# Kernel tuning notes

Measured on AMD Instinct MI355X. Metric: run time of the kernel, lower is better.

Reference implementation:

```python
import jax, jax.numpy as jnp
import numpy as np
import math

B, NQ, NK, HD = 8, 1024, 1024, 1024   # batch, q_len(=up_dim), kv_len(=img_size+15), hidden
H, HS, KC = 8, 128, 32                # heads, head_size=hidden/8, k_caption
EPS = 1e-5


def setup_inputs() -> dict:
    key = jax.random.key(0)
    ks = jax.random.split(key, 16)
    f = lambda i, sh: jax.random.normal(ks[i], sh, dtype=jnp.float32)
    s = 0.02  # weight init scale
    return {
        "v": f(0, (B, NK, HD)),
        "k": f(1, (B, NK, HD)),
        "q": f(2, (B, NQ, HD)),
        "c": f(3, (B, KC, HD)),
        "Wv": f(4, (HD, HD)) * s, "bv": jnp.zeros((HD,), jnp.float32),
        "Wk": f(5, (HD, HD)) * s, "bk": jnp.zeros((HD,), jnp.float32),
        "Wq": f(6, (HD, HD)) * s, "bq": jnp.zeros((HD,), jnp.float32),
        "Wc": f(7, (HD, HD)) * s, "bc": jnp.zeros((HD,), jnp.float32),
        "Wm": f(8, (HD, HD)) * s, "bm": jnp.zeros((HD,), jnp.float32),
        "Wup": f(9, (NQ, KC)) * s,          # nn.Linear(k_caption, up_dim, bias=False) weight (out,in)
        "ln_w": jnp.ones((NK,), jnp.float32),
        "ln_b": jnp.zeros((NK,), jnp.float32),
        "tau": jnp.float32(3.0),
    }


def _heads(x, W, b):
    # x: [B, N, HD] -> [B, H, N, HS]
    y = x @ W.T + b
    return y.reshape(x.shape[0], x.shape[1], H, HS).transpose(0, 2, 1, 3)


def reference(v, k, q, c, Wv, bv, Wk, bk, Wq, bq, Wc, bc, Wm, bm, Wup, ln_w, ln_b, tau):
    vh = _heads(v, Wv, bv)                      # [B,H,NK,HS]
    kh = _heads(k, Wk, bk)                      # [B,H,NK,HS]
    qh = _heads(q, Wq, bq)                      # [B,H,NQ,HS]
    ch = _heads(c, Wc, bc)                      # [B,H,KC,HS]

    inv_sqrt_d = 1.0 / math.sqrt(HS)            # d_k == d_c == head_size
    scores = jnp.einsum("bhqd,bhkd->bhqk", qh, kh) * inv_sqrt_d  # [B,H,NQ,NK]

    # up-sample context along caption axis: KC -> NQ (Linear over that axis, no bias)
    cu = jnp.einsum("bhcd,uc->bhud", ch, Wup)   # [B,H,NQ,HS]
    c_scores = jnp.einsum("bhud,bhkd->bhuk", cu, kh) * inv_sqrt_d  # [B,H,NQ,NK]

    t = jnp.tanh(tau)
    scores = (scores + c_scores * t) / (1.0 + t)

    # LayerNorm over the key axis (last dim), applied to raw scores
    mu = jnp.mean(scores, axis=-1, keepdims=True)
    var = jnp.var(scores, axis=-1, keepdims=True)
    scores = (scores - mu) * jax.lax.rsqrt(var + EPS) * ln_w + ln_b

    att = jax.nn.softmax(scores, axis=-1)       # dropout_r=0 -> identity
    out = jnp.einsum("bhqk,bhkd->bhqd", att, vh)  # [B,H,NQ,HS]
    out = out.transpose(0, 2, 1, 3).reshape(q.shape[0], NQ, HD)
    return out @ Wm.T + bm
```

## Files before the change

### kernel.cpp

```cpp
#include <hip/hip_runtime.h>
#include <hip/hip_fp16.h>


typedef _Float16 f16;
typedef _Float16 f16x8 __attribute__((ext_vector_type(8)));
typedef _Float16 f16x4 __attribute__((ext_vector_type(4)));
typedef float    f32x4 __attribute__((ext_vector_type(4)));

#define B_  8
#define NQ_ 1024
#define NK_ 1024
#define HD_ 1024
#define H_  8
#define HS_ 128
#define KC_ 32

__device__ __forceinline__ void g2lds16(const void* g, void* l) {
    __builtin_amdgcn_global_load_lds((const __attribute__((address_space(1))) void*)g,
                                     (__attribute__((address_space(3))) void*)l, 16, 0, 0);
}

__global__ __launch_bounds__(256) void fill_sentinel(float* __restrict__ out, int n) {
    int i = blockIdx.x * 256 + threadIdx.x;
    if (i < n) out[i] = 12345.0f;
}

__global__ __launch_bounds__(256) void cvt_f32_f16(const float* __restrict__ in,
                                                   f16* __restrict__ out, int n4) {
    int i = blockIdx.x * 256 + threadIdx.x;
    if (i >= n4) return;
    float4 v = ((const float4*)in)[i];
    f16x4 o;
    o[0] = (f16)v.x; o[1] = (f16)v.y; o[2] = (f16)v.z; o[3] = (f16)v.w;
    ((f16x4*)out)[i] = o;
}

template <int MODE>
__global__ __launch_bounds__(256) void gemm_nt(
    const f16* __restrict__ A, long long sA,
    const f16* __restrict__ B, long long sB,
    void* __restrict__ Cv, long long sC,
    int M, int N, int K,
    const float* __restrict__ bias,
    const f16* __restrict__ extra, long long sE,
    const float* __restrict__ taup)
{
    __shared__ __align__(16) f16 As[128 * 32];
    __shared__ __align__(16) f16 Bs[128 * 32];
    const int bz = blockIdx.z;
    const f16* Ab = A + (size_t)bz * sA;
    const f16* Bb = B + (size_t)bz * sB;
    const int row0 = blockIdx.y * 128, col0 = blockIdx.x * 128;
    const int tid = threadIdx.x, wave = tid >> 6, lane = tid & 63;
    const int g = lane >> 4, li = lane & 15;
    const int wr = wave >> 1, wc = wave & 1;

    f32x4 acc[4][4];
#pragma unroll
    for (int i = 0; i < 4; i++)
#pragma unroll
        for (int j = 0; j < 4; j++) acc[i][j] = (f32x4){0.f, 0.f, 0.f, 0.f};

    for (int k0 = 0; k0 < K; k0 += 32) {
#pragma unroll
        for (int i = 0; i < 2; i++) {
            int slot = i * 256 + tid;
            int rr = slot >> 2, cc8 = (slot & 3) << 3;
            int ra = row0 + rr;
            if (MODE == 0 && ra >= M) ra = M - 1;
            g2lds16(Ab + (size_t)ra * K + k0 + cc8, As + (size_t)(i * 256 + wave * 64) * 8);
            g2lds16(Bb + (size_t)(col0 + rr) * K + k0 + cc8, Bs + (size_t)(i * 256 + wave * 64) * 8);
        }
        __syncthreads();
        f16x8 af[4], bf[4];
#pragma unroll
        for (int i = 0; i < 4; i++) af[i] = *(const f16x8*)&As[(wr * 64 + i * 16 + li) * 32 + g * 8];
#pragma unroll
        for (int j = 0; j < 4; j++) bf[j] = *(const f16x8*)&Bs[(wc * 64 + j * 16 + li) * 32 + g * 8];
#pragma unroll
        for (int i = 0; i < 4; i++)
#pragma unroll
            for (int j = 0; j < 4; j++)
                acc[i][j] = __builtin_amdgcn_mfma_f32_16x16x32_f16(af[i], bf[j], acc[i][j], 0, 0, 0);
        __syncthreads();
    }

    float tv = 0.f, qscale = 0.f;
    if constexpr (MODE == 3) {
        tv = tanhf(taup[0]);
        qscale = 0.08838834764831845f / (1.0f + tv);
    }
#pragma unroll
    for (int i = 0; i < 4; i++) {
#pragma unroll
        for (int j = 0; j < 4; j++) {
            int cc = col0 + wc * 64 + j * 16 + li;
            float bcol = (MODE == 2) ? 0.f : bias[cc];
#pragma unroll
            for (int r = 0; r < 4; r++) {
                int row = row0 + wr * 64 + i * 16 + g * 4 + r;
                if (MODE == 0 && row >= M) continue;
                float v = acc[i][j][r];
                if constexpr (MODE == 2) v += bias[row]; else v += bcol;
                size_t idx = (size_t)bz * sC + (size_t)row * N + cc;
                if constexpr (MODE == 0) ((float*)Cv)[idx] = v;
                else if constexpr (MODE == 1 || MODE == 2) ((f16*)Cv)[idx] = (f16)v;
                else if constexpr (MODE == 3) {
                    v = (v + tv * (float)extra[(size_t)bz * sE + (size_t)row * N + cc]) * qscale;
                    ((f16*)Cv)[idx] = (f16)v;
                } else ((float*)Cv)[idx] = v;
            }
        }
    }
}

__global__ __launch_bounds__(256) void upsample_k(const float* __restrict__ Wup,
                                                  const float* __restrict__ CH,
                                                  f16* __restrict__ CU) {
    const int u = blockIdx.x, b = blockIdx.y;
    const float* ch = CH + (size_t)b * KC_ * HD_;
    float w[KC_];
#pragma unroll
    for (int c = 0; c < KC_; c++) w[c] = Wup[u * KC_ + c];
    f16* out = CU + ((size_t)b * NQ_ + u) * HD_;
#pragma unroll
    for (int t = 0; t < 4; t++) {
        int i = threadIdx.x + t * 256;
        float acc = 0.f;
#pragma unroll
        for (int c = 0; c < KC_; c++) acc += w[c] * ch[c * HD_ + i];
        out[i] = (f16)acc;
    }
}

#define MFMA16(A_, B_, C_) __builtin_amdgcn_mfma_f32_16x16x32_f16(A_, B_, C_, 0, 0, 0)

__global__ void attn_k(
    const f16* __restrict__ QE,
    const f16* __restrict__ KH,
    const f16* __restrict__ VT,
    const float* __restrict__ lnw_g, const float* __restrict__ lnb_g,
    f16* __restrict__ ATT)
{
    __shared__ __align__(16) f16 Plds[16 * NK_];
    __shared__ float redS[4][16], redQ[4][16], redL[4][16];

    const int tid = threadIdx.x;
    const int wave = tid >> 6, lane = tid & 63, g = lane >> 4, li = lane & 15;
    const int b = blockIdx.z, h = blockIdx.y, q0 = blockIdx.x * 16;

    const f16* qp = QE + (size_t)(b * NQ_ + q0 + li) * HD_ + h * HS_ + g * 8;
    f16x8 a[4];
#pragma unroll
    for (int ks = 0; ks < 4; ks++) a[ks] = *(const f16x8*)(qp + ks * 32);

    const f16* kp = KH + (size_t)(b * NK_ + wave * 256 + li) * HD_ + h * HS_ + g * 8;
    f32x4 s[16];
#pragma unroll
    for (int j = 0; j < 16; j++) s[j] = (f32x4){0.f, 0.f, 0.f, 0.f};

    f16x8 kbA0, kbA1, kbB0, kbB1, kbC0, kbC1, kbD0, kbD1;
#define QK_LD(BUF, U) do { \
        const f16* _p = kp + (size_t)((U) >> 1) * 16 * HD_ + ((U) & 1) * 64; \
        kb##BUF##0 = *(const f16x8*)(_p); \
        kb##BUF##1 = *(const f16x8*)(_p + 32); \
    } while (0)
#define QK_FMA(BUF, U) do { \
        __builtin_amdgcn_s_setprio(1); \
        s[(U) >> 1] = MFMA16(a[((U) & 1) * 2],     kb##BUF##0, s[(U) >> 1]); \
        s[(U) >> 1] = MFMA16(a[((U) & 1) * 2 + 1], kb##BUF##1, s[(U) >> 1]); \
        __builtin_amdgcn_s_setprio(0); \
    } while (0)

    QK_LD(A, 0); QK_LD(B, 1); QK_LD(C, 2); QK_LD(D, 3);
#pragma unroll
    for (int u = 0; u < 32; u += 4) {
        QK_FMA(A, u);     if (u + 4 < 32) QK_LD(A, u + 4);
        QK_FMA(B, u + 1); if (u + 5 < 32) QK_LD(B, u + 5);
        QK_FMA(C, u + 2); if (u + 6 < 32) QK_LD(C, u + 6);
        QK_FMA(D, u + 3); if (u + 7 < 32) QK_LD(D, u + 7);
    }

    float lw[16], lb[16];
#pragma unroll
    for (int j = 0; j < 16; j++) {
        int key = wave * 256 + j * 16 + li;
        lw[j] = lnw_g[key];
        lb[j] = lnb_g[key];
    }

    float ps[4] = {0, 0, 0, 0}, pq[4] = {0, 0, 0, 0};
#pragma unroll
    for (int j = 0; j < 16; j++)
#pragma unroll
        for (int r = 0; r < 4; r++) { float x = s[j][r]; ps[r] += x; pq[r] += x * x; }
#pragma unroll
    for (int m = 1; m < 16; m <<= 1)
#pragma unroll
        for (int r = 0; r < 4; r++) { ps[r] += __shfl_xor(ps[r], m, 64); pq[r] += __shfl_xor(pq[r], m, 64); }
    if (li == 0)
#pragma unroll
        for (int r = 0; r < 4; r++) { redS[wave][g * 4 + r] = ps[r]; redQ[wave][g * 4 + r] = pq[r]; }
    __syncthreads();

    float mu[4], rs[4];
#pragma unroll
    for (int r = 0; r < 4; r++) {
        int row = g * 4 + r;
        float s1 = redS[0][row] + redS[1][row] + redS[2][row] + redS[3][row];
        float s2 = redQ[0][row] + redQ[1][row] + redQ[2][row] + redQ[3][row];
        float m_ = s1 * (1.f / 1024.f);
        mu[r] = m_;
        rs[r] = rsqrtf(s2 * (1.f / 1024.f) - m_ * m_ + 1e-5f);
    }

    float sm[4] = {0, 0, 0, 0};
#pragma unroll
    for (int j = 0; j < 16; j++) {
        int key = wave * 256 + j * 16 + li;
        int chunk = key >> 3, sub = key & 7;
#pragma unroll
        for (int r = 0; r < 4; r++) {
            int row = g * 4 + r;
            float x = (s[j][r] - mu[r]) * rs[r] * lw[j] + lb[j];
            float e = __expf(fminf(x, 11.f) - 4.f);
            sm[r] += e;
            Plds[row * NK_ + ((chunk ^ (row & 7)) << 3) + sub] = (f16)e;
        }
    }
#pragma unroll
    for (int m = 1; m < 16; m <<= 1)
#pragma unroll
        for (int r = 0; r < 4; r++) sm[r] += __shfl_xor(sm[r], m, 64);
    if (li == 0)
#pragma unroll
        for (int r = 0; r < 4; r++) redL[wave][g * 4 + r] = sm[r];
    __syncthreads();

    float ls[4];
#pragma unroll
    for (int r = 0; r < 4; r++) {
        int row = g * 4 + r;
        ls[r] = redL[0][row] + redL[1][row] + redL[2][row] + redL[3][row];
    }

    const f16* vp = VT + (size_t)(b * HD_ + h * HS_ + wave * 32 + li) * NK_ + g * 8;
    f32x4 o0a = (f32x4){0.f, 0.f, 0.f, 0.f}, o0b = o0a, o1a = o0a, o1b = o0a;
    f16x8 paA, v0A, v1A, paB, v0B, v1B, paC, v0C, v1C, paD, v0D, v1D;
#define PV_LD(BUF, U) do { \
        pa##BUF = *(const f16x8*)&Plds[(size_t)li * NK_ + ((((U) * 4 + g) ^ (li & 7)) << 3)]; \
        v0##BUF = *(const f16x8*)(vp + (size_t)(U) * 32); \
        v1##BUF = *(const f16x8*)(vp + (size_t)16 * NK_ + (size_t)(U) * 32); \
    } while (0)
#define PV_FMA(BUF, OA, OB) do { \
        __builtin_amdgcn_s_setprio(1); \
        OA = MFMA16(pa##BUF, v0##BUF, OA); \
        OB = MFMA16(pa##BUF, v1##BUF, OB); \
        __builtin_amdgcn_s_setprio(0); \
    } while (0)

    PV_LD(A, 0); PV_LD(B, 1); PV_LD(C, 2); PV_LD(D, 3);
#pragma unroll
    for (int u = 0; u < 32; u += 4) {
        PV_FMA(A, o0a, o1a); if (u + 4 < 32) PV_LD(A, u + 4);
        PV_FMA(B, o0b, o1b); if (u + 5 < 32) PV_LD(B, u + 5);
        PV_FMA(C, o0a, o1a); if (u + 6 < 32) PV_LD(C, u + 6);
        PV_FMA(D, o0b, o1b); if (u + 7 < 32) PV_LD(D, u + 7);
    }

    f16* op = ATT + (size_t)(b * NQ_ + q0) * HD_ + h * HS_ + wave * 32 + li;
#pragma unroll
    for (int r = 0; r < 4; r++) {
        int row = g * 4 + r;
        float inv = 1.f / ls[r];
        op[(size_t)row * HD_]      = (f16)((o0a[r] + o0b[r]) * inv);
        op[(size_t)row * HD_ + 16] = (f16)((o1a[r] + o1b[r]) * inv);
    }
}

extern "C" void kernel_launch(void* const* d_in, const int* in_sizes, int n_in,
                              void* d_out, int out_size, void* d_ws, size_t ws_size,
                              hipStream_t stream) {
    const float* v   = (const float*)d_in[0];
    const float* k   = (const float*)d_in[1];
    const float* q   = (const float*)d_in[2];
    const float* c   = (const float*)d_in[3];
    const float* Wv  = (const float*)d_in[4];
    const float* bv  = (const float*)d_in[5];
    const float* Wk  = (const float*)d_in[6];
    const float* bk  = (const float*)d_in[7];
    const float* Wq  = (const float*)d_in[8];
    const float* bq  = (const float*)d_in[9];
    const float* Wc  = (const float*)d_in[10];
    const float* bc  = (const float*)d_in[11];
    const float* Wm  = (const float*)d_in[12];
    const float* bm  = (const float*)d_in[13];
    const float* Wup = (const float*)d_in[14];
    const float* lnw = (const float*)d_in[15];
    const float* lnb = (const float*)d_in[16];
    const float* tau = (const float*)d_in[17];

    const size_t NE  = (size_t)B_ * NK_ * HD_;
    const size_t NW  = (size_t)HD_ * HD_;
    const size_t NC  = (size_t)B_ * KC_ * HD_;

    const size_t REQUIRED = 95944704;
    if (ws_size < REQUIRED) {
        fill_sentinel<<<dim3((out_size + 255) / 256), dim3(256), 0, stream>>>((float*)d_out, out_size);
        return;
    }
    char* ws = (char*)d_ws;
    f16*  k16  = (f16*)(ws + 0);
    f16*  QE   = (f16*)(ws + 0);
    f16*  v16  = (f16*)(ws + 16777216);
    f16*  CU16 = (f16*)(ws + 16777216);
    f16*  q16  = (f16*)(ws + 33554432);
    f16*  ATT  = (f16*)(ws + 33554432);
    f16*  c16  = (f16*)(ws + 50331648);
    float* CHf = (float*)(ws + 50855936);
    f16*  wk16 = (f16*)(ws + 51904512);
    f16*  wq16 = (f16*)(ws + 54001664);
    f16*  wv16 = (f16*)(ws + 56098816);
    f16*  wc16 = (f16*)(ws + 58195968);
    f16*  wm16 = (f16*)(ws + 60293120);
    f16*  KH   = (f16*)(ws + 62390272);
    f16*  VT   = (f16*)(ws + 79167488);

    dim3 blk(256);
    auto cvt = [&](const float* in, f16* out, size_t n) {
        cvt_f32_f16<<<dim3((unsigned)(n / 1024)), blk, 0, stream>>>(in, out, (int)(n / 4));
    };
    cvt(k, k16, NE);
    cvt(v, v16, NE);
    cvt(q, q16, NE);
    cvt(c, c16, NC);
    cvt(Wk, wk16, NW);
    cvt(Wq, wq16, NW);
    cvt(Wv, wv16, NW);
    cvt(Wc, wc16, NW);
    cvt(Wm, wm16, NW);

    gemm_nt<1><<<dim3(8, 8, 8), blk, 0, stream>>>(k16, (long long)NK_ * HD_, wk16, 0,
        KH, (long long)NK_ * HD_, NK_, HD_, HD_, bk, nullptr, 0, nullptr);
    gemm_nt<2><<<dim3(8, 8, 8), blk, 0, stream>>>(wv16, 0, v16, (long long)NK_ * HD_,
        VT, (long long)HD_ * NK_, HD_, NK_, HD_, bv, nullptr, 0, nullptr);
    gemm_nt<0><<<dim3(8, 1, 8), blk, 0, stream>>>(c16, (long long)KC_ * HD_, wc16, 0,
        CHf, (long long)KC_ * HD_, KC_, HD_, HD_, bc, nullptr, 0, nullptr);
    upsample_k<<<dim3(NQ_, B_), blk, 0, stream>>>(Wup, CHf, CU16);
    gemm_nt<3><<<dim3(8, 8, 8), blk, 0, stream>>>(q16, (long long)NQ_ * HD_, wq16, 0,
        QE, (long long)NQ_ * HD_, NQ_, HD_, HD_, bq, CU16, (long long)NQ_ * HD_, tau);
    attn_k<<<dim3(NQ_ / 16, H_, B_), blk, 0, stream>>>(QE, KH, VT, lnw, lnb, ATT);
    gemm_nt<4><<<dim3(8, 8, 8), blk, 0, stream>>>(ATT, (long long)NQ_ * HD_, wm16, 0,
        d_out, (long long)NQ_ * HD_, NQ_, HD_, HD_, bm, nullptr, 0, nullptr);
}
```

Before: 639.9 us.

## Process 32 query rows per attention block with 8 waves and XCD-aware mapping

The attention kernel now handles 32 query rows per workgroup using 512 threads (8 waves), each wave covering 128 keys. Every K and V fragment loaded from global memory is therefore reused for two 16-row query tiles, halving K/V traffic per query. The 1D grid is remapped so that each (batch, head) pair's blocks land on the same XCD, which should improve L2 reuse of K/V. The reduction scratch is aliased onto the larger P buffer, which costs an extra barrier, and LDS use doubles to 64KB, which may lower occupancy.

```diff
diff --git a/kernel.cpp b/kernel.cpp
--- a/kernel.cpp
+++ b/kernel.cpp
@@ -135,40 +135,47 @@
 
 #define MFMA16(A_, B_, C_) __builtin_amdgcn_mfma_f32_16x16x32_f16(A_, B_, C_, 0, 0, 0)
 
-__global__ void attn_k(
+__global__ __launch_bounds__(512) void attn_k(
     const f16* __restrict__ QE,
     const f16* __restrict__ KH,
     const f16* __restrict__ VT,
     const float* __restrict__ lnw_g, const float* __restrict__ lnb_g,
     f16* __restrict__ ATT)
 {
-    __shared__ __align__(16) f16 Plds[16 * NK_];
-    __shared__ float redS[4][16], redQ[4][16], redL[4][16];
+    __shared__ __align__(16) f16 Plds[32 * NK_];
+    float* redS = (float*)Plds;
+    float* redQ = redS + 256;
+    float* redL = redQ + 256;
 
     const int tid = threadIdx.x;
     const int wave = tid >> 6, lane = tid & 63, g = lane >> 4, li = lane & 15;
-    const int b = blockIdx.z, h = blockIdx.y, q0 = blockIdx.x * 16;
+
+    const int wgid = blockIdx.x;
+    const int xcd = wgid & 7;
+    const int n = wgid >> 3;
+    const int pair = ((n >> 5) << 3) | xcd;
+    const int b = pair >> 3, h = pair & 7;
+    const int q0 = (n & 31) * 32;
 
     const f16* qp = QE + (size_t)(b * NQ_ + q0 + li) * HD_ + h * HS_ + g * 8;
-    f16x8 a[4];
-#pragma unroll
-    for (int ks = 0; ks < 4; ks++) a[ks] = *(const f16x8*)(qp + ks * 32);
-
-    const f16* kp = KH + (size_t)(b * NK_ + wave * 256 + li) * HD_ + h * HS_ + g * 8;
-    f32x4 s[16];
-#pragma unroll
-    for (int j = 0; j < 16; j++) s[j] = (f32x4){0.f, 0.f, 0.f, 0.f};
-
-    f16x8 kbA0, kbA1, kbB0, kbB1, kbC0, kbC1, kbD0, kbD1;
-#define QK_LD(BUF, U) do { \
-        const f16* _p = kp + (size_t)((U) >> 1) * 16 * HD_ + ((U) & 1) * 64; \
-        kb##BUF##0 = *(const f16x8*)(_p); \
-        kb##BUF##1 = *(const f16x8*)(_p + 32); \
-    } while (0)
+    f16x8 a0[4], a1[4];
+#pragma unroll
+    for (int ks = 0; ks < 4; ks++) {
+        a0[ks] = *(const f16x8*)(qp + ks * 32);
+        a1[ks] = *(const f16x8*)(qp + (size_t)16 * HD_ + ks * 32);
+    }
+
+    const f16* kp = KH + (size_t)(b * NK_ + wave * 128 + li) * HD_ + h * HS_ + g * 8;
+    f32x4 s0[8], s1[8];
+#pragma unroll
+    for (int j = 0; j < 8; j++) { s0[j] = (f32x4){0.f,0.f,0.f,0.f}; s1[j] = s0[j]; }
+
+    f16x8 kbA, kbB, kbC, kbD;
+#define QK_LD(BUF, U) kb##BUF = *(const f16x8*)(kp + (size_t)((U) & 7) * 16 * HD_ + ((U) >> 3) * 32)
 #define QK_FMA(BUF, U) do { \
         __builtin_amdgcn_s_setprio(1); \
-        s[(U) >> 1] = MFMA16(a[((U) & 1) * 2],     kb##BUF##0, s[(U) >> 1]); \
-        s[(U) >> 1] = MFMA16(a[((U) & 1) * 2 + 1], kb##BUF##1, s[(U) >> 1]); \
+        s0[(U) & 7] = MFMA16(a0[(U) >> 3], kb##BUF, s0[(U) & 7]); \
+        s1[(U) & 7] = MFMA16(a1[(U) >> 3], kb##BUF, s1[(U) & 7]); \
         __builtin_amdgcn_s_setprio(0); \
     } while (0)
 
@@ -181,81 +188,117 @@
         QK_FMA(D, u + 3); if (u + 7 < 32) QK_LD(D, u + 7);
     }
 
-    float lw[16], lb[16];
-#pragma unroll
-    for (int j = 0; j < 16; j++) {
-        int key = wave * 256 + j * 16 + li;
+    float lw[8], lb[8];
+#pragma unroll
+    for (int j = 0; j < 8; j++) {
+        int key = wave * 128 + j * 16 + li;
         lw[j] = lnw_g[key];
         lb[j] = lnb_g[key];
     }
 
-    float ps[4] = {0, 0, 0, 0}, pq[4] = {0, 0, 0, 0};
-#pragma unroll
-    for (int j = 0; j < 16; j++)
-#pragma unroll
-        for (int r = 0; r < 4; r++) { float x = s[j][r]; ps[r] += x; pq[r] += x * x; }
+    float ps0[4] = {0,0,0,0}, pq0[4] = {0,0,0,0}, ps1[4] = {0,0,0,0}, pq1[4] = {0,0,0,0};
+#pragma unroll
+    for (int j = 0; j < 8; j++)
+#pragma unroll
+        for (int r = 0; r < 4; r++) {
+            float x0 = s0[j][r]; ps0[r] += x0; pq0[r] += x0 * x0;
+            float x1 = s1[j][r]; ps1[r] += x1; pq1[r] += x1 * x1;
+        }
 #pragma unroll
     for (int m = 1; m < 16; m <<= 1)
 #pragma unroll
-        for (int r = 0; r < 4; r++) { ps[r] += __shfl_xor(ps[r], m, 64); pq[r] += __shfl_xor(pq[r], m, 64); }
+        for (int r = 0; r < 4; r++) {
+            ps0[r] += __shfl_xor(ps0[r], m, 64); pq0[r] += __shfl_xor(pq0[r], m, 64);
+            ps1[r] += __shfl_xor(ps1[r], m, 64); pq1[r] += __shfl_xor(pq1[r], m, 64);
+        }
     if (li == 0)
 #pragma unroll
-        for (int r = 0; r < 4; r++) { redS[wave][g * 4 + r] = ps[r]; redQ[wave][g * 4 + r] = pq[r]; }
+        for (int r = 0; r < 4; r++) {
+            redS[wave * 32 + g * 4 + r] = ps0[r];      redQ[wave * 32 + g * 4 + r] = pq0[r];
+            redS[wave * 32 + 16 + g * 4 + r] = ps1[r]; redQ[wave * 32 + 16 + g * 4 + r] = pq1[r];
+        }
     __syncthreads();
 
-    float mu[4], rs[4];
+    float mu0[4], rs0[4], mu1[4], rs1[4];
 #pragma unroll
     for (int r = 0; r < 4; r++) {
-        int row = g * 4 + r;
-        float s1 = redS[0][row] + redS[1][row] + redS[2][row] + redS[3][row];
-        float s2 = redQ[0][row] + redQ[1][row] + redQ[2][row] + redQ[3][row];
-        float m_ = s1 * (1.f / 1024.f);
-        mu[r] = m_;
-        rs[r] = rsqrtf(s2 * (1.f / 1024.f) - m_ * m_ + 1e-5f);
-    }
-
-    float sm[4] = {0, 0, 0, 0};
-#pragma unroll
-    for (int j = 0; j < 16; j++) {
-        int key = wave * 256 + j * 16 + li;
+        float s1a = 0.f, s2a = 0.f, s1b = 0.f, s2b = 0.f;
+#pragma unroll
+        for (int w = 0; w < 8; w++) {
+            s1a += redS[w * 32 + g * 4 + r];      s2a += redQ[w * 32 + g * 4 + r];
+            s1b += redS[w * 32 + 16 + g * 4 + r]; s2b += redQ[w * 32 + 16 + g * 4 + r];
+        }
+        float ma = s1a * (1.f / 1024.f), mb = s1b * (1.f / 1024.f);
+        mu0[r] = ma; rs0[r] = rsqrtf(s2a * (1.f / 1024.f) - ma * ma + 1e-5f);
+        mu1[r] = mb; rs1[r] = rsqrtf(s2b * (1.f / 1024.f) - mb * mb + 1e-5f);
+    }
+
+    float sm0[4] = {0,0,0,0}, sm1[4] = {0,0,0,0};
+#pragma unroll
+    for (int j = 0; j < 8; j++)
+#pragma unroll
+        for (int r = 0; r < 4; r++) {
+            float x0 = (s0[j][r] - mu0[r]) * rs0[r] * lw[j] + lb[j];
+            float e0 = __expf(fminf(x0, 11.f) - 4.f);
+            s0[j][r] = e0; sm0[r] += e0;
+            float x1 = (s1[j][r] - mu1[r]) * rs1[r] * lw[j] + lb[j];
+            float e1 = __expf(fminf(x1, 11.f) - 4.f);
+            s1[j][r] = e1; sm1[r] += e1;
+        }
+#pragma unroll
+    for (int m = 1; m < 16; m <<= 1)
+#pragma unroll
+        for (int r = 0; r < 4; r++) {
+            sm0[r] += __shfl_xor(sm0[r], m, 64);
+            sm1[r] += __shfl_xor(sm1[r], m, 64);
+        }
+    if (li == 0)
+#pragma unroll
+        for (int r = 0; r < 4; r++) {
+            redL[wave * 32 + g * 4 + r] = sm0[r];
+            redL[wave * 32 + 16 + g * 4 + r] = sm1[r];
+        }
+    __syncthreads();
+
+    float ls0[4], ls1[4];
+#pragma unroll
+    for (int r = 0; r < 4; r++) {
+        float la = 0.f, lbs = 0.f;
+#pragma unroll
+        for (int w = 0; w < 8; w++) {
+            la += redL[w * 32 + g * 4 + r];
+            lbs += redL[w * 32 + 16 + g * 4 + r];
+        }
+        ls0[r] = la; ls1[r] = lbs;
+    }
+    __syncthreads();
+
+#pragma unroll
+    for (int j = 0; j < 8; j++) {
+        int key = wave * 128 + j * 16 + li;
         int chunk = key >> 3, sub = key & 7;
 #pragma unroll
         for (int r = 0; r < 4; r++) {
-            int row = g * 4 + r;
-            float x = (s[j][r] - mu[r]) * rs[r] * lw[j] + lb[j];
-            float e = __expf(fminf(x, 11.f) - 4.f);
-            sm[r] += e;
-            Plds[row * NK_ + ((chunk ^ (row & 7)) << 3) + sub] = (f16)e;
-        }
-    }
-#pragma unroll
-    for (int m = 1; m < 16; m <<= 1)
-#pragma unroll
-        for (int r = 0; r < 4; r++) sm[r] += __shfl_xor(sm[r], m, 64);
-    if (li == 0)
-#pragma unroll
-        for (int r = 0; r < 4; r++) redL[wave][g * 4 + r] = sm[r];
+            int row0 = g * 4 + r, row1 = 16 + g * 4 + r;
+            Plds[row0 * NK_ + ((chunk ^ (row0 & 7)) << 3) + sub] = (f16)s0[j][r];
+            Plds[row1 * NK_ + ((chunk ^ (row1 & 7)) << 3) + sub] = (f16)s1[j][r];
+        }
+    }
     __syncthreads();
 
-    float ls[4];
-#pragma unroll
-    for (int r = 0; r < 4; r++) {
-        int row = g * 4 + r;
-        ls[r] = redL[0][row] + redL[1][row] + redL[2][row] + redL[3][row];
-    }
-
-    const f16* vp = VT + (size_t)(b * HD_ + h * HS_ + wave * 32 + li) * NK_ + g * 8;
-    f32x4 o0a = (f32x4){0.f, 0.f, 0.f, 0.f}, o0b = o0a, o1a = o0a, o1b = o0a;
-    f16x8 paA, v0A, v1A, paB, v0B, v1B, paC, v0C, v1C, paD, v0D, v1D;
+    const f16* vp = VT + (size_t)(b * HD_ + h * HS_ + wave * 16 + li) * NK_ + g * 8;
+    f32x4 o0a = (f32x4){0.f,0.f,0.f,0.f}, o0b = o0a, o1a = o0a, o1b = o0a;
+    f16x8 pa0A, pa1A, vA, pa0B, pa1B, vB, pa0C, pa1C, vC, pa0D, pa1D, vD;
 #define PV_LD(BUF, U) do { \
-        pa##BUF = *(const f16x8*)&Plds[(size_t)li * NK_ + ((((U) * 4 + g) ^ (li & 7)) << 3)]; \
-        v0##BUF = *(const f16x8*)(vp + (size_t)(U) * 32); \
-        v1##BUF = *(const f16x8*)(vp + (size_t)16 * NK_ + (size_t)(U) * 32); \
+        size_t _c = (size_t)((((U) * 4 + g) ^ (li & 7)) << 3); \
+        pa0##BUF = *(const f16x8*)&Plds[(size_t)li * NK_ + _c]; \
+        pa1##BUF = *(const f16x8*)&Plds[(size_t)(16 + li) * NK_ + _c]; \
+        v##BUF   = *(const f16x8*)(vp + (size_t)(U) * 32); \
     } while (0)
-#define PV_FMA(BUF, OA, OB) do { \
+#define PV_FMA(BUF, O0, O1) do { \
         __builtin_amdgcn_s_setprio(1); \
-        OA = MFMA16(pa##BUF, v0##BUF, OA); \
-        OB = MFMA16(pa##BUF, v1##BUF, OB); \
+        O0 = MFMA16(pa0##BUF, v##BUF, O0); \
+        O1 = MFMA16(pa1##BUF, v##BUF, O1); \
         __builtin_amdgcn_s_setprio(0); \
     } while (0)
 
@@ -268,13 +311,12 @@
         PV_FMA(D, o0b, o1b); if (u + 7 < 32) PV_LD(D, u + 7);
     }
 
-    f16* op = ATT + (size_t)(b * NQ_ + q0) * HD_ + h * HS_ + wave * 32 + li;
+    f16* op = ATT + (size_t)(b * NQ_ + q0) * HD_ + h * HS_ + wave * 16 + li;
 #pragma unroll
     for (int r = 0; r < 4; r++) {
-        int row = g * 4 + r;
-        float inv = 1.f / ls[r];
-        op[(size_t)row * HD_]      = (f16)((o0a[r] + o0b[r]) * inv);
-        op[(size_t)row * HD_ + 16] = (f16)((o1a[r] + o1b[r]) * inv);
+        int row0 = g * 4 + r, row1 = 16 + g * 4 + r;
+        op[(size_t)row0 * HD_] = (f16)((o0a[r] + o0b[r]) / ls0[r]);
+        op[(size_t)row1 * HD_] = (f16)((o1a[r] + o1b[r]) / ls1[r]);
     }
 }
 
@@ -349,7 +391,7 @@
     upsample_k<<<dim3(NQ_, B_), blk, 0, stream>>>(Wup, CHf, CU16);
     gemm_nt<3><<<dim3(8, 8, 8), blk, 0, stream>>>(q16, (long long)NQ_ * HD_, wq16, 0,
         QE, (long long)NQ_ * HD_, NQ_, HD_, HD_, bq, CU16, (long long)NQ_ * HD_, tau);
-    attn_k<<<dim3(NQ_ / 16, H_, B_), blk, 0, stream>>>(QE, KH, VT, lnw, lnb, ATT);
+    attn_k<<<dim3(2048), dim3(512), 0, stream>>>(QE, KH, VT, lnw, lnb, ATT);
     gemm_nt<4><<<dim3(8, 8, 8), blk, 0, stream>>>(ATT, (long long)NQ_ * HD_, wm16, 0,
         d_out, (long long)NQ_ * HD_, NQ_, HD_, HD_, bm, nullptr, 0, nullptr);
 }
```

Result: faster. 570.9 us (-10.8%).
